# Optimization experiments

Measured on AMD Instinct MI355X. Metric: run time of the kernel, lower is better.

The kernel has to match this reference:

```python
import jax, jax.numpy as jnp
import numpy as np

B, S, D = 4, 8192, 512
H, DK = 8, 64
LOCAL_W = 256
GLOBAL_STRIDE = 64
LN_EPS = 1e-5


def setup_inputs() -> dict:
    key = jax.random.key(0)
    ks = jax.random.split(key, 9)
    scale = 1.0 / np.sqrt(D)
    def lin(k, din, dout):
        return jax.random.normal(k, (din, dout), jnp.float32) * scale
    return {
        "x": jax.random.normal(ks[0], (B, S, D), jnp.float32),
        "lq_w": lin(ks[1], D, D), "lq_b": jnp.zeros((D,), jnp.float32),
        "lk_w": lin(ks[2], D, D), "lk_b": jnp.zeros((D,), jnp.float32),
        "lv_w": lin(ks[3], D, D), "lv_b": jnp.zeros((D,), jnp.float32),
        "gq_w": lin(ks[4], D, D), "gq_b": jnp.zeros((D,), jnp.float32),
        "gk_w": lin(ks[5], D, D), "gk_b": jnp.zeros((D,), jnp.float32),
        "gv_w": lin(ks[6], D, D), "gv_b": jnp.zeros((D,), jnp.float32),
        "out_w": jax.random.normal(ks[7], (2 * D, D), jnp.float32) * (1.0 / np.sqrt(2 * D)),
        "out_b": jnp.zeros((D,), jnp.float32),
        "ln_g": jnp.ones((D,), jnp.float32),
        "ln_b": jnp.zeros((D,), jnp.float32),
    }


def _local_attention(x, qw, qb, kw, kb, vw, vb):
    # x: [B,S,D]; S divisible by LOCAL_W -> no padding path.
    nW = S // LOCAL_W
    xw = x.reshape(B, nW, LOCAL_W, D)
    def heads(w, b):
        y = jnp.einsum('bnwd,de->bnwe', xw, w) + b  # [B,nW,W,D]
        return y.reshape(B, nW, LOCAL_W, H, DK).transpose(0, 1, 3, 2, 4)  # [B,nW,H,W,dk]
    q, k, v = heads(qw, qb), heads(kw, kb), heads(vw, vb)
    scores = jnp.einsum('bnhqd,bnhkd->bnhqk', q, k) / np.sqrt(DK)
    attn = jax.nn.softmax(scores, axis=-1)
    out = jnp.einsum('bnhqk,bnhkd->bnhqd', attn, v)  # [B,nW,H,W,dk]
    return out.transpose(0, 1, 3, 2, 4).reshape(B, S, D)


def _global_attention(x, qw, qb, kw, kb, vw, vb):
    gc = x[:, ::GLOBAL_STRIDE]                       # [B,G,D]
    G = gc.shape[1]
    q = (x @ qw + qb).reshape(B, S, H, DK)           # [B,S,H,dk]
    k = (gc @ kw + kb).reshape(B, G, H, DK)
    v = (gc @ vw + vb).reshape(B, G, H, DK)
    scores = jnp.einsum('bshd,bghd->bhsg', q, k) / np.sqrt(DK)
    attn = jax.nn.softmax(scores, axis=-1)
    out = jnp.einsum('bhsg,bghd->bshd', attn, v)
    return out.reshape(B, S, D)


def reference(x, lq_w, lq_b, lk_w, lk_b, lv_w, lv_b,
              gq_w, gq_b, gk_w, gk_b, gv_w, gv_b,
              out_w, out_b, ln_g, ln_b):
    local = _local_attention(x, lq_w, lq_b, lk_w, lk_b, lv_w, lv_b)
    glob = _global_attention(x, gq_w, gq_b, gk_w, gk_b, gv_w, gv_b)
    combined = jnp.concatenate([local, glob], axis=-1) @ out_w + out_b
    h = x + combined  # dropout is identity in eval
    mu = jnp.mean(h, axis=-1, keepdims=True)
    var = jnp.var(h, axis=-1, keepdims=True)
    return (h - mu) / jnp.sqrt(var + LN_EPS) * ln_g + ln_b
```

## Files before the change

### kernel.cpp

```cpp
#include <hip/hip_runtime.h>
#include <hip/hip_bf16.h>
#include <stdint.h>

#define B_ 4
#define S_ 8192
#define D_ 512
#define H_ 8
#define DK_ 64
#define G_ 128
#define ROWS_ (B_*S_)

typedef unsigned short u16;
typedef __attribute__((ext_vector_type(8))) short short8;
typedef __attribute__((ext_vector_type(4))) short short4v;
typedef __attribute__((ext_vector_type(4))) float floatx4;

static __device__ __forceinline__ float bf2f(u16 u){
  union { uint32_t i; float f; } v; v.i = ((uint32_t)u) << 16; return v.f;
}
static __device__ __forceinline__ u16 f2bf(float f){
  union { float f; uint32_t i; } v; v.f = f;
  uint32_t u = v.i; u += 0x7fff + ((u >> 16) & 1); return (u16)(u >> 16);
}

static __device__ __forceinline__ void glds16(const u16* g, u16* l){
  __builtin_amdgcn_global_load_lds(
      (const __attribute__((address_space(1))) void*)g,
      (__attribute__((address_space(3))) void*)l, 16, 0, 0);
}

__global__ void cast_x_kernel(const float* __restrict__ x, u16* __restrict__ xb,
                              u16* __restrict__ xg, int n4){
  int i = blockIdx.x*blockDim.x + threadIdx.x;
  if (i >= n4) return;
  float4 v = ((const float4*)x)[i];
  short4v o;
  o[0] = (short)f2bf(v.x); o[1] = (short)f2bf(v.y);
  o[2] = (short)f2bf(v.z); o[3] = (short)f2bf(v.w);
  *(short4v*)(xb + (size_t)i*4) = o;
  int row = i >> 7;
  if ((row & 63) == 0){
    int b = row >> 13, g = (row & 8191) >> 6;
    *(short4v*)(xg + ((size_t)(b*G_ + g)*D_) + (i & 127)*4) = o;
  }
}

__global__ void transpose_cast_kernel(const float* __restrict__ W, u16* __restrict__ Ot, int K, int N){
  __shared__ float t[64][65];
  int n0 = blockIdx.x*64, k0 = blockIdx.y*64;
  int tx = threadIdx.x & 63, ty = threadIdx.x >> 6;
#pragma unroll
  for (int j=0;j<16;j++){ int k = ty + j*4; t[k][tx] = W[(size_t)(k0+k)*N + n0+tx]; }
  __syncthreads();
#pragma unroll
  for (int j=0;j<16;j++){ int n = ty + j*4; Ot[(size_t)(n0+n)*K + k0 + tx] = f2bf(t[tx][n]); }
}

__global__ void transpose_cast6_kernel(const float* s0, const float* s1, const float* s2,
    const float* s3, const float* s4, const float* s5,
    u16* __restrict__ WcatT, u16* __restrict__ WgT){
  __shared__ float t[64][65];
  int z = blockIdx.z;
  const float* W = (z==0)?s0:(z==1)?s1:(z==2)?s2:(z==3)?s3:(z==4)?s4:s5;
  u16* Ot = (z<4) ? (WcatT + (size_t)z*512*512) : (WgT + (size_t)(z-4)*512*512);
  int n0 = blockIdx.x*64, k0 = blockIdx.y*64;
  int tx = threadIdx.x & 63, ty = threadIdx.x >> 6;
#pragma unroll
  for (int j=0;j<16;j++){ int k = ty + j*4; t[k][tx] = W[(size_t)(k0+k)*512 + n0+tx]; }
  __syncthreads();
#pragma unroll
  for (int j=0;j<16;j++){ int n = ty + j*4; Ot[(size_t)(n0+n)*512 + k0 + tx] = f2bf(t[tx][n]); }
}

__global__ void build_bias_kernel(float* __restrict__ bcat, float* __restrict__ bg,
    const float* lq_b, const float* lk_b, const float* lv_b, const float* gq_b,
    const float* gk_b, const float* gv_b){
  int i = blockIdx.x*blockDim.x + threadIdx.x;
  if (i < 2048){
    const float* s = (i < 512) ? lq_b : (i < 1024) ? lk_b : (i < 1536) ? lv_b : gq_b;
    bcat[i] = s[i & 511];
  } else if (i < 3072){
    int j = i - 2048;
    bg[j] = (j < 512) ? gk_b[j] : gv_b[j - 512];
  }
}

template<int EPI>
__global__ __launch_bounds__(512, 1) void gemm_big(
    const u16* __restrict__ A, const u16* __restrict__ Bt,
    const float* __restrict__ bias, u16* __restrict__ C,
    const u16* __restrict__ X, int M, int N, int K)
{
  __shared__ u16 SM[4][16384];
  const int tid = threadIdx.x, lane = tid & 63, w = tid >> 6;
  const int wm = w >> 2, wn = w & 3;
  const int gx = gridDim.x;
  const int h = blockIdx.y * gx + blockIdx.x;
  const int chunk = (gx * gridDim.y) >> 3;
  const int work = (h & 7) * chunk + (h >> 3);
  const int bx = work % gx, by = work / gx;
  const int m0 = by*256, n0 = bx*256;
  const int T = K >> 5;

  const u16* gsrc[4]; int loff[4];
#pragma unroll
  for (int j = 0; j < 4; j++){
    int fb  = w*4 + j;
    int isB = fb >> 4;
    int blk = fb & 15;
    const u16* bp = isB ? Bt : A;
    int row = (isB ? n0 : m0) + blk*16 + (lane & 15);
    gsrc[j] = bp + (size_t)row * K + ((lane >> 4) * 8);
    loff[j] = fb*512;
  }

  floatx4 acc[8][4] = {};

#pragma unroll
  for (int tt = 0; tt < 3; tt++)
#pragma unroll
    for (int j = 0; j < 4; j++)
      glds16(gsrc[j] + tt*32, &SM[tt][loff[j]]);

#pragma unroll 4
  for (int t = 0; t < T; t++){
    if (t <= T - 3)      asm volatile("s_waitcnt vmcnt(8)" ::: "memory");
    else if (t == T - 2) asm volatile("s_waitcnt vmcnt(4)" ::: "memory");
    else                 asm volatile("s_waitcnt vmcnt(0)" ::: "memory");
    __builtin_amdgcn_s_barrier();

    if (t + 3 < T){
      u16* Sb = &SM[(t + 3) & 3][0];
#pragma unroll
      for (int j = 0; j < 4; j++) glds16(gsrc[j] + (t+3)*32, Sb + loff[j]);
    }

    const u16* Tb = &SM[t & 3][0];
    short8 aR[8], bR[4];
#pragma unroll
    for (int i=0;i<8;i++) aR[i] = *(const short8*)(Tb + (wm*8 + i)*512 + lane*8);
#pragma unroll
    for (int j=0;j<4;j++) bR[j] = *(const short8*)(Tb + (16 + wn*4 + j)*512 + lane*8);
#pragma unroll
    for (int i=0;i<8;i++)
#pragma unroll
      for (int j=0;j<4;j++)
        acc[i][j] = __builtin_amdgcn_mfma_f32_16x16x32_bf16(aR[i], bR[j], acc[i][j], 0,0,0);
  }

#pragma unroll
  for (int mi=0; mi<8; mi++)
#pragma unroll
    for (int nj=0; nj<4; nj++){
      int col = n0 + (wn*4 + nj)*16 + (lane & 15);
      float bv = bias[col];
#pragma unroll
      for (int ii=0; ii<4; ii++){
        size_t row = (size_t)(m0 + (wm*8 + mi)*16 + (lane>>4)*4 + ii);
        float v = acc[mi][nj][ii] + bv;
        if (EPI == 1) v += bf2f(X[row*N + col]);
        C[row*N + col] = f2bf(v);
      }
    }
}

__global__ __launch_bounds__(256) void gemm_small(
    const u16* __restrict__ A, const u16* __restrict__ Bt,
    const float* __restrict__ bias, u16* __restrict__ C,
    int M, int N, int K)
{
  __shared__ u16 As[128*32];
  __shared__ u16 Bs[128*32];
  const int tid = threadIdx.x, lane = tid & 63, w = tid >> 6;
  const int m0 = blockIdx.y*128, n0 = blockIdx.x*128;
  const int wm = (w>>1)*64, wn = (w&1)*64;
  floatx4 acc[4][4] = {};
  const int c0 = 2*w;
  const int sr = lane >> 2;
  const int sc = (lane & 3) * 8;
  const u16* ga0 = A  + (size_t)(m0 +  c0     *16 + sr)*K + sc;
  const u16* ga1 = A  + (size_t)(m0 + (c0 + 1)*16 + sr)*K + sc;
  const u16* gb0 = Bt + (size_t)(n0 +  c0     *16 + sr)*K + sc;
  const u16* gb1 = Bt + (size_t)(n0 + (c0 + 1)*16 + sr)*K + sc;
  u16* la0 = &As[ c0     *512];
  u16* la1 = &As[(c0 + 1)*512];
  u16* lb0 = &Bs[ c0     *512];
  u16* lb1 = &Bs[(c0 + 1)*512];

  for (int k0 = 0; k0 < K; k0 += 32){
    __syncthreads();
    glds16(ga0 + k0, la0);
    glds16(ga1 + k0, la1);
    glds16(gb0 + k0, lb0);
    glds16(gb1 + k0, lb1);
    __syncthreads();
    short8 af[4], bf[4];
#pragma unroll
    for (int i=0;i<4;i++) af[i] = *(const short8*)&As[(wm + i*16 + (lane&15))*32 + (lane>>4)*8];
#pragma unroll
    for (int i=0;i<4;i++) bf[i] = *(const short8*)&Bs[(wn + i*16 + (lane&15))*32 + (lane>>4)*8];
#pragma unroll
    for (int mi=0;mi<4;mi++)
#pragma unroll
      for (int ni=0;ni<4;ni++)
        acc[mi][ni] = __builtin_amdgcn_mfma_f32_16x16x32_bf16(af[mi], bf[ni], acc[mi][ni], 0,0,0);
  }

#pragma unroll
  for (int mi=0;mi<4;mi++)
#pragma unroll
    for (int ni=0;ni<4;ni++){
      int col = n0 + wn + ni*16 + (lane&15);
      float bv = bias[col];
#pragma unroll
      for (int i=0;i<4;i++){
        size_t row = (size_t)(m0 + wm + mi*16 + (lane>>4)*4 + i);
        C[row*N + col] = f2bf(acc[mi][ni][i] + bv);
      }
    }
}

template<int KVLEN, int KSTRIDE, bool GLOBAL>
__global__ __launch_bounds__(512, 2) void attn_kernel(
    const u16* __restrict__ qkv, const u16* __restrict__ kvbuf, u16* __restrict__ comb)
{
  __shared__ u16 SM[KVLEN*256];
  u16* Kl = SM;
  u16* Vt = SM + KVLEN*64;
  u16* Pl = SM + KVLEN*128;
  const int tid = threadIdx.x, lane = tid & 63, w = tid >> 6;
  const int h = blockIdx.x, n = blockIdx.y, b = blockIdx.z;
  const size_t qrow0 = (size_t)b*S_ + (size_t)n*256;
  const int krow0 = GLOBAL ? b*G_ : (b*S_ + n*256);
  const int qc = (GLOBAL ? 1536 : 0)   + h*DK_;
  const int kc = (GLOBAL ? 0    : 512) + h*DK_;
  const int vc = (GLOBAL ? 512  : 1024)+ h*DK_;
  const int oc = (GLOBAL ? 512  : 0)   + h*DK_;
  constexpr int NF = KVLEN/16;

  {
    const int rpw = KVLEN/8;
    const int r0w = w * rpw;
    const int cg = ((lane & 7) ^ (lane >> 3)) * 8;
    const int rl = lane >> 3;
#pragma unroll
    for (int j = 0; j < rpw; j += 8){
      int row = r0w + j + rl;
      glds16(kvbuf + (size_t)(krow0 + row)*KSTRIDE + kc + cg, &Kl[(r0w + j)*64]);
    }
  }
  if (tid < (KVLEN/4)*8){
    const int rb = tid >> 3;
    const int kv0 = rb * 4;
    const int d0 = (tid & 7) * 8;
    const u16* vp = kvbuf + (size_t)(krow0 + kv0)*KSTRIDE + vc + d0;
    short8 rIn[4];
#pragma unroll
    for (int i=0;i<4;i++) rIn[i] = *(const short8*)(vp + (size_t)i*KSTRIDE);
    const int c   = rb >> 1;
    const int sub = kv0 & 7;
#pragma unroll
    for (int dd=0; dd<8; dd++){
      int d = d0 + dd;
      short4v o;
#pragma unroll
      for (int j=0;j<4;j++) o[j] = rIn[j][dd];
      *(short4v*)&Vt[d*KVLEN + ((c ^ (d&7)) << 3) + sub] = o;
    }
  }
  __syncthreads();

  const float sc2 = 0.125f * 1.44269504f;
  const int Pbase = w*16*KVLEN;

  for (int sp = 2*w; sp < 2*w + 2; sp++){
    const u16* qp = qkv + (qrow0 + sp*16 + (lane&15))*2048 + qc + ((lane>>4)*8);
    short8 qf0 = *(const short8*)qp;
    short8 qf1 = *(const short8*)(qp + 32);

    floatx4 sacc[NF];
#pragma unroll
    for (int nf = 0; nf < NF; nf++){
      const u16* kb = &Kl[(nf*16 + (lane&15))*64];
      short8 kf0 = *(const short8*)(kb + ((( lane>>4)      ^ (lane&7)) << 3));
      short8 kf1 = *(const short8*)(kb + ((((lane>>4) + 4) ^ (lane&7)) << 3));
      floatx4 z = {0.f,0.f,0.f,0.f};
      z = __builtin_amdgcn_mfma_f32_16x16x32_bf16(qf0, kf0, z, 0,0,0);
      z = __builtin_amdgcn_mfma_f32_16x16x32_bf16(qf1, kf1, z, 0,0,0);
      sacc[nf] = z;
    }

    float sm[4] = {0.f,0.f,0.f,0.f};
#pragma unroll
    for (int nf=0;nf<NF;nf++)
#pragma unroll
      for (int i=0;i<4;i++){
        float e = exp2f(sacc[nf][i] * sc2);
        sacc[nf][i] = e; sm[i] += e;
      }
#pragma unroll
    for (int i=0;i<4;i++){
#pragma unroll
      for (int msk=1; msk<16; msk<<=1) sm[i] += __shfl_xor(sm[i], msk);
      sm[i] = 1.f / sm[i];
    }

#pragma unroll
    for (int nf=0;nf<NF;nf++)
#pragma unroll
      for (int i=0;i<4;i++){
        int row = (lane>>4)*4 + i;
        int ch  = nf*2 + ((lane>>3)&1);
        Pl[Pbase + row*KVLEN + ((ch ^ (row&7)) << 3) + (lane&7)] = f2bf(sacc[nf][i]*sm[i]);
      }

    floatx4 oacc[4] = {};
#pragma unroll
    for (int kk=0; kk<KVLEN/32; kk++){
      int prow = lane & 15;
      short8 pf = *(const short8*)&Pl[Pbase + prow*KVLEN + (((kk*4 + (lane>>4)) ^ (prow&7)) << 3)];
#pragma unroll
      for (int nd=0; nd<4; nd++){
        int d = nd*16 + (lane&15);
        short8 vf = *(const short8*)&Vt[d*KVLEN + (((kk*4 + (lane>>4)) ^ (d&7)) << 3)];
        oacc[nd] = __builtin_amdgcn_mfma_f32_16x16x32_bf16(pf, vf, oacc[nd], 0,0,0);
      }
    }

#pragma unroll
    for (int nd=0; nd<4; nd++)
#pragma unroll
      for (int i=0;i<4;i++){
        size_t row = qrow0 + sp*16 + (lane>>4)*4 + i;
        comb[row*1024 + oc + nd*16 + (lane&15)] = f2bf(oacc[nd][i]);
      }
  }
}

__global__ __launch_bounds__(256) void ln_kernel(const u16* __restrict__ hb,
    float* __restrict__ out, const float* __restrict__ g, const float* __restrict__ bta){
  int lane = threadIdx.x & 63, w = threadIdx.x >> 6;
  size_t row = (size_t)blockIdx.x*4 + w;
  const u16* p = hb + row*D_;
  short8 hv = *(const short8*)(p + lane*8);
  float f[8]; float s = 0.f, q = 0.f;
#pragma unroll
  for (int i=0;i<8;i++){ f[i] = bf2f((u16)hv[i]); s += f[i]; q += f[i]*f[i]; }
#pragma unroll
  for (int msk=1; msk<64; msk<<=1){ s += __shfl_xor(s, msk); q += __shfl_xor(q, msk); }
  float mean = s * (1.f/512.f);
  float var  = q * (1.f/512.f) - mean*mean;
  float inv  = rsqrtf(var + 1e-5f);
  float4 g0 = ((const float4*)g)[lane*2],   g1 = ((const float4*)g)[lane*2+1];
  float4 b0 = ((const float4*)bta)[lane*2], b1 = ((const float4*)bta)[lane*2+1];
  float4 o0, o1;
  o0.x = (f[0]-mean)*inv*g0.x + b0.x; o0.y = (f[1]-mean)*inv*g0.y + b0.y;
  o0.z = (f[2]-mean)*inv*g0.z + b0.z; o0.w = (f[3]-mean)*inv*g0.w + b0.w;
  o1.x = (f[4]-mean)*inv*g1.x + b1.x; o1.y = (f[5]-mean)*inv*g1.y + b1.y;
  o1.z = (f[6]-mean)*inv*g1.z + b1.z; o1.w = (f[7]-mean)*inv*g1.w + b1.w;
  float* op = out + row*D_;
  ((float4*)op)[lane*2]     = o0;
  ((float4*)op)[lane*2 + 1] = o1;
}

extern "C" void kernel_launch(void* const* d_in, const int* in_sizes, int n_in,
                              void* d_out, int out_size, void* d_ws, size_t ws_size,
                              hipStream_t stream)
{
  const float* x    = (const float*)d_in[0];
  const float* lq_w = (const float*)d_in[1];
  const float* lq_b = (const float*)d_in[2];
  const float* lk_w = (const float*)d_in[3];
  const float* lk_b = (const float*)d_in[4];
  const float* lv_w = (const float*)d_in[5];
  const float* lv_b = (const float*)d_in[6];
  const float* gq_w = (const float*)d_in[7];
  const float* gq_b = (const float*)d_in[8];
  const float* gk_w = (const float*)d_in[9];
  const float* gk_b = (const float*)d_in[10];
  const float* gv_w = (const float*)d_in[11];
  const float* gv_b = (const float*)d_in[12];
  const float* out_w = (const float*)d_in[13];
  const float* out_b = (const float*)d_in[14];
  const float* ln_g = (const float*)d_in[15];
  const float* ln_b = (const float*)d_in[16];

  char* ws = (char*)d_ws;
  size_t off = 0;
  auto alloc = [&](size_t bytes)->void*{ void* p = ws + off; off += (bytes + 255) & ~255ULL; return p; };
  u16*  xb    = (u16*) alloc((size_t)ROWS_*D_*2);
  u16*  xg    = (u16*) alloc((size_t)512*512*2);
  u16*  WcatT = (u16*) alloc((size_t)2048*512*2);
  u16*  WgT   = (u16*) alloc((size_t)1024*512*2);
  u16*  WoutT = (u16*) alloc((size_t)512*1024*2);
  float* bcat = (float*)alloc(2048*4);
  float* bg   = (float*)alloc(1024*4);
  u16*  qkvg  = (u16*) alloc((size_t)ROWS_*2048*2);
  u16*  gkv   = (u16*) alloc((size_t)512*1024*2);
  u16*  comb  = (u16*) alloc((size_t)ROWS_*1024*2);
  u16*  hbuf  = qkvg;

  cast_x_kernel<<<16384,256,0,stream>>>(x, xb, xg, ROWS_*D_/4);
  transpose_cast6_kernel<<<dim3(8,8,6),256,0,stream>>>(lq_w, lk_w, lv_w, gq_w, gk_w, gv_w, WcatT, WgT);
  transpose_cast_kernel<<<dim3(8,16),256,0,stream>>>(out_w, WoutT, 1024, 512);
  build_bias_kernel<<<12,256,0,stream>>>(bcat, bg, lq_b, lk_b, lv_b, gq_b, gk_b, gv_b);

  gemm_big<0><<<dim3(8,128),512,0,stream>>>(xb, WcatT, bcat, qkvg, nullptr, ROWS_, 2048, 512);
  gemm_small<<<dim3(8,4),256,0,stream>>>(xg, WgT, bg, gkv, 512, 1024, 512);

  attn_kernel<256,2048,false><<<dim3(8,32,4),512,0,stream>>>(qkvg, qkvg, comb);
  attn_kernel<128,1024,true ><<<dim3(8,32,4),512,0,stream>>>(qkvg, gkv,  comb);

  gemm_big<1><<<dim3(2,128),512,0,stream>>>(comb, WoutT, out_b, hbuf, xb,
      ROWS_, 512, 1024);
  ln_kernel<<<8192,256,0,stream>>>(hbuf, (float*)d_out, ln_g, ln_b);
}
```

Measured before the change: 275.7 us.

## Chunk attention KV into 128-row halves, halve query rows per block, defer normalization

The attention kernel now handles 128 query rows per block, one 16-row slice per wave, and doubles the grid. Keys and values are streamed in 128-row chunks with a fixed 64KB shared buffer. Softmax normalization is deferred: unnormalized exponentials feed the PV MFMA and the row sum is applied once at the end, without max subtraction (as before). This cuts LDS per block and register pressure to allow four blocks per SM, at the cost of reloading local-window K/V twice per window and an extra barrier per chunk.

```diff
diff --git a/kernel.cpp b/kernel.cpp
--- a/kernel.cpp
+++ b/kernel.cpp
@@ -220,67 +220,66 @@
     }
 }
 
-template<int KVLEN, int KSTRIDE, bool GLOBAL>
-__global__ __launch_bounds__(512, 2) void attn_kernel(
+template<int NHALF, int KSTRIDE, bool GLOBAL>
+__global__ __launch_bounds__(512, 4) void attn_kernel(
     const u16* __restrict__ qkv, const u16* __restrict__ kvbuf, u16* __restrict__ comb)
 {
-  __shared__ u16 SM[KVLEN*256];
+  __shared__ u16 SM[32768];
   u16* Kl = SM;
-  u16* Vt = SM + KVLEN*64;
-  u16* Pl = SM + KVLEN*128;
+  u16* Vt = SM + 8192;
+  u16* Pl = SM + 16384;
   const int tid = threadIdx.x, lane = tid & 63, w = tid >> 6;
-  const int h = blockIdx.x, n = blockIdx.y, b = blockIdx.z;
-  const size_t qrow0 = (size_t)b*S_ + (size_t)n*256;
-  const int krow0 = GLOBAL ? b*G_ : (b*S_ + n*256);
+  const int h = blockIdx.x, yy = blockIdx.y, b = blockIdx.z;
+  const size_t qrow0 = (size_t)b*S_ + (size_t)yy*128;
+  const int krow0 = GLOBAL ? b*G_ : (b*S_ + (yy>>1)*256);
   const int qc = (GLOBAL ? 1536 : 0)   + h*DK_;
   const int kc = (GLOBAL ? 0    : 512) + h*DK_;
   const int vc = (GLOBAL ? 512  : 1024)+ h*DK_;
   const int oc = (GLOBAL ? 512  : 0)   + h*DK_;
-  constexpr int NF = KVLEN/16;
-
-  {
-    const int rpw = KVLEN/8;
-    const int r0w = w * rpw;
-    const int cg = ((lane & 7) ^ (lane >> 3)) * 8;
-    const int rl = lane >> 3;
-#pragma unroll
-    for (int j = 0; j < rpw; j += 8){
-      int row = r0w + j + rl;
-      glds16(kvbuf + (size_t)(krow0 + row)*KSTRIDE + kc + cg, &Kl[(r0w + j)*64]);
-    }
-  }
-  if (tid < (KVLEN/4)*8){
-    const int rb = tid >> 3;
-    const int kv0 = rb * 4;
-    const int d0 = (tid & 7) * 8;
-    const u16* vp = kvbuf + (size_t)(krow0 + kv0)*KSTRIDE + vc + d0;
-    short8 rIn[4];
-#pragma unroll
-    for (int i=0;i<4;i++) rIn[i] = *(const short8*)(vp + (size_t)i*KSTRIDE);
-    const int c   = rb >> 1;
-    const int sub = kv0 & 7;
-#pragma unroll
-    for (int dd=0; dd<8; dd++){
-      int d = d0 + dd;
-      short4v o;
-#pragma unroll
-      for (int j=0;j<4;j++) o[j] = rIn[j][dd];
-      *(short4v*)&Vt[d*KVLEN + ((c ^ (d&7)) << 3) + sub] = o;
-    }
-  }
-  __syncthreads();
-
+
+  const u16* qp = qkv + (qrow0 + w*16 + (lane&15))*2048 + qc + ((lane>>4)*8);
+  short8 qf0 = *(const short8*)qp;
+  short8 qf1 = *(const short8*)(qp + 32);
+
+  floatx4 oacc[4] = {};
+  float smv[4] = {0.f,0.f,0.f,0.f};
   const float sc2 = 0.125f * 1.44269504f;
-  const int Pbase = w*16*KVLEN;
-
-  for (int sp = 2*w; sp < 2*w + 2; sp++){
-    const u16* qp = qkv + (qrow0 + sp*16 + (lane&15))*2048 + qc + ((lane>>4)*8);
-    short8 qf0 = *(const short8*)qp;
-    short8 qf1 = *(const short8*)(qp + 32);
-
-    floatx4 sacc[NF];
-#pragma unroll
-    for (int nf = 0; nf < NF; nf++){
+  const int Pbase = w*16*128;
+  const int cg = ((lane & 7) ^ (lane >> 3)) * 8;
+  const int rl = lane >> 3;
+
+#pragma unroll
+  for (int hh = 0; hh < NHALF; hh++){
+    if (hh) __syncthreads();
+    {
+      const int r0w = w*16;
+      glds16(kvbuf + (size_t)(krow0 + hh*128 + r0w + rl)*KSTRIDE + kc + cg, &Kl[r0w*64]);
+      glds16(kvbuf + (size_t)(krow0 + hh*128 + r0w + 8 + rl)*KSTRIDE + kc + cg, &Kl[(r0w + 8)*64]);
+    }
+    if (tid < 256){
+      const int rb = tid >> 3;
+      const int kv0 = rb * 4;
+      const int d0 = (tid & 7) * 8;
+      const u16* vp = kvbuf + (size_t)(krow0 + hh*128 + kv0)*KSTRIDE + vc + d0;
+      short8 rIn[4];
+#pragma unroll
+      for (int i=0;i<4;i++) rIn[i] = *(const short8*)(vp + (size_t)i*KSTRIDE);
+      const int c   = rb >> 1;
+      const int sub = kv0 & 7;
+#pragma unroll
+      for (int dd=0; dd<8; dd++){
+        int d = d0 + dd;
+        short4v o;
+#pragma unroll
+        for (int j=0;j<4;j++) o[j] = rIn[j][dd];
+        *(short4v*)&Vt[d*128 + ((c ^ (d&7)) << 3) + sub] = o;
+      }
+    }
+    __syncthreads();
+
+    floatx4 sacc[8];
+#pragma unroll
+    for (int nf = 0; nf < 8; nf++){
       const u16* kb = &Kl[(nf*16 + (lane&15))*64];
       short8 kf0 = *(const short8*)(kb + ((( lane>>4)      ^ (lane&7)) << 3));
       short8 kf1 = *(const short8*)(kb + ((((lane>>4) + 4) ^ (lane&7)) << 3));
@@ -289,52 +288,42 @@
       z = __builtin_amdgcn_mfma_f32_16x16x32_bf16(qf1, kf1, z, 0,0,0);
       sacc[nf] = z;
     }
-
-    float sm[4] = {0.f,0.f,0.f,0.f};
-#pragma unroll
-    for (int nf=0;nf<NF;nf++)
+#pragma unroll
+    for (int nf=0;nf<8;nf++)
 #pragma unroll
       for (int i=0;i<4;i++){
         float e = exp2f(sacc[nf][i] * sc2);
-        sacc[nf][i] = e; sm[i] += e;
-      }
-#pragma unroll
-    for (int i=0;i<4;i++){
-#pragma unroll
-      for (int msk=1; msk<16; msk<<=1) sm[i] += __shfl_xor(sm[i], msk);
-      sm[i] = 1.f / sm[i];
-    }
-
-#pragma unroll
-    for (int nf=0;nf<NF;nf++)
-#pragma unroll
-      for (int i=0;i<4;i++){
+        smv[i] += e;
         int row = (lane>>4)*4 + i;
         int ch  = nf*2 + ((lane>>3)&1);
-        Pl[Pbase + row*KVLEN + ((ch ^ (row&7)) << 3) + (lane&7)] = f2bf(sacc[nf][i]*sm[i]);
+        Pl[Pbase + row*128 + ((ch ^ (row&7)) << 3) + (lane&7)] = f2bf(e);
       }
-
-    floatx4 oacc[4] = {};
-#pragma unroll
-    for (int kk=0; kk<KVLEN/32; kk++){
+#pragma unroll
+    for (int kk=0; kk<4; kk++){
       int prow = lane & 15;
-      short8 pf = *(const short8*)&Pl[Pbase + prow*KVLEN + (((kk*4 + (lane>>4)) ^ (prow&7)) << 3)];
+      short8 pf = *(const short8*)&Pl[Pbase + prow*128 + (((kk*4 + (lane>>4)) ^ (prow&7)) << 3)];
 #pragma unroll
       for (int nd=0; nd<4; nd++){
         int d = nd*16 + (lane&15);
-        short8 vf = *(const short8*)&Vt[d*KVLEN + (((kk*4 + (lane>>4)) ^ (d&7)) << 3)];
+        short8 vf = *(const short8*)&Vt[d*128 + (((kk*4 + (lane>>4)) ^ (d&7)) << 3)];
         oacc[nd] = __builtin_amdgcn_mfma_f32_16x16x32_bf16(pf, vf, oacc[nd], 0,0,0);
       }
     }
-
-#pragma unroll
-    for (int nd=0; nd<4; nd++)
-#pragma unroll
-      for (int i=0;i<4;i++){
-        size_t row = qrow0 + sp*16 + (lane>>4)*4 + i;
-        comb[row*1024 + oc + nd*16 + (lane&15)] = f2bf(oacc[nd][i]);
-      }
-  }
+  }
+
+#pragma unroll
+  for (int i=0;i<4;i++){
+#pragma unroll
+    for (int msk=1; msk<16; msk<<=1) smv[i] += __shfl_xor(smv[i], msk);
+    smv[i] = 1.f / smv[i];
+  }
+#pragma unroll
+  for (int nd=0; nd<4; nd++)
+#pragma unroll
+    for (int i=0;i<4;i++){
+      size_t row = qrow0 + w*16 + (lane>>4)*4 + i;
+      comb[row*1024 + oc + nd*16 + (lane&15)] = f2bf(oacc[nd][i] * smv[i]);
+    }
 }
 
 __global__ __launch_bounds__(256) void ln_kernel(const u16* __restrict__ hb,
@@ -408,8 +397,8 @@
   gemm_big<0><<<dim3(8,128),512,0,stream>>>(xb, WcatT, bcat, qkvg, nullptr, ROWS_, 2048, 512);
   gemm_small<<<dim3(8,4),256,0,stream>>>(xg, WgT, bg, gkv, 512, 1024, 512);
 
-  attn_kernel<256,2048,false><<<dim3(8,32,4),512,0,stream>>>(qkvg, qkvg, comb);
-  attn_kernel<128,1024,true ><<<dim3(8,32,4),512,0,stream>>>(qkvg, gkv,  comb);
+  attn_kernel<2,2048,false><<<dim3(8,64,4),512,0,stream>>>(qkvg, qkvg, comb);
+  attn_kernel<1,1024,true ><<<dim3(8,64,4),512,0,stream>>>(qkvg, gkv,  comb);
 
   gemm_big<1><<<dim3(2,128),512,0,stream>>>(comb, WoutT, out_b, hbuf, xb,
       ROWS_, 512, 1024);
```

After: 282.7 us. 1.03x slower.

## Double-buffer LDS fragment reads in GEMM main loop to overlap with MFMA

Applied to the files above, without the earlier changes.

Restructures the GEMM K-loop into a two-step unrolled loop with two register fragment sets. Fragments for the next K-slice are read from shared memory while MFMAs run on the current slice, so LDS latency can hide behind matrix math. The waitcnt and barrier schedule is reworked to match. This raises register pressure (two fragment sets alongside the 8x4 accumulators) and assumes T is even.

```diff
diff --git a/kernel.cpp b/kernel.cpp
--- a/kernel.cpp
+++ b/kernel.cpp
@@ -116,36 +116,47 @@
 
   floatx4 acc[8][4] = {};
 
-#pragma unroll
-  for (int tt = 0; tt < 3; tt++)
-#pragma unroll
-    for (int j = 0; j < 4; j++)
-      glds16(gsrc[j] + tt*32, &SM[tt][loff[j]]);
-
-#pragma unroll 4
-  for (int t = 0; t < T; t++){
-    if (t <= T - 3)      asm volatile("s_waitcnt vmcnt(8)" ::: "memory");
-    else if (t == T - 2) asm volatile("s_waitcnt vmcnt(4)" ::: "memory");
-    else                 asm volatile("s_waitcnt vmcnt(0)" ::: "memory");
+  auto stageT = [&](int tt){
+    u16* Sb_ = &SM[tt & 3][0];
+#pragma unroll
+    for (int j = 0; j < 4; j++) glds16(gsrc[j] + tt*32, Sb_ + loff[j]);
+  };
+  auto readFrags = [&](short8* Sa, short8* Sb, int slot){
+    const u16* Tb = &SM[slot][0];
+#pragma unroll
+    for (int i=0;i<8;i++) Sa[i] = *(const short8*)(Tb + (wm*8 + i)*512 + lane*8);
+#pragma unroll
+    for (int j=0;j<4;j++) Sb[j] = *(const short8*)(Tb + (16 + wn*4 + j)*512 + lane*8);
+  };
+  auto doMfma = [&](const short8* Sa, const short8* Sb){
+#pragma unroll
+    for (int i=0;i<8;i++)
+#pragma unroll
+      for (int j=0;j<4;j++)
+        acc[i][j] = __builtin_amdgcn_mfma_f32_16x16x32_bf16(Sa[i], Sb[j], acc[i][j], 0,0,0);
+  };
+
+  short8 A0[8], B0[4], A1[8], B1[4];
+
+  stageT(0); stageT(1); stageT(2);
+  asm volatile("s_waitcnt vmcnt(8)" ::: "memory");
+  __builtin_amdgcn_s_barrier();
+  readFrags(A0, B0, 0);
+
+  for (int t = 0; t < T; t += 2){
+    if (t + 2 < T) asm volatile("s_waitcnt vmcnt(4)" ::: "memory");
+    else           asm volatile("s_waitcnt vmcnt(0)" ::: "memory");
     __builtin_amdgcn_s_barrier();
-
-    if (t + 3 < T){
-      u16* Sb = &SM[(t + 3) & 3][0];
-#pragma unroll
-      for (int j = 0; j < 4; j++) glds16(gsrc[j] + (t+3)*32, Sb + loff[j]);
-    }
-
-    const u16* Tb = &SM[t & 3][0];
-    short8 aR[8], bR[4];
-#pragma unroll
-    for (int i=0;i<8;i++) aR[i] = *(const short8*)(Tb + (wm*8 + i)*512 + lane*8);
-#pragma unroll
-    for (int j=0;j<4;j++) bR[j] = *(const short8*)(Tb + (16 + wn*4 + j)*512 + lane*8);
-#pragma unroll
-    for (int i=0;i<8;i++)
-#pragma unroll
-      for (int j=0;j<4;j++)
-        acc[i][j] = __builtin_amdgcn_mfma_f32_16x16x32_bf16(aR[i], bR[j], acc[i][j], 0,0,0);
+    if (t + 3 < T) stageT(t + 3);
+    readFrags(A1, B1, (t + 1) & 3);
+    doMfma(A0, B0);
+
+    if (t + 3 < T) asm volatile("s_waitcnt vmcnt(4)" ::: "memory");
+    else           asm volatile("s_waitcnt vmcnt(0)" ::: "memory");
+    __builtin_amdgcn_s_barrier();
+    if (t + 4 < T) stageT(t + 4);
+    if (t + 2 < T) readFrags(A0, B0, (t + 2) & 3);
+    doMfma(A1, B1);
   }
 
 #pragma unroll
```

Measured after the change: 277.0 us. No clear change (+0.5%).
